# Optimization experiments

Hardware: AMD Instinct MI355X
Metric: run time of the kernel (lower is better)

The kernel has to match this reference:

```python
import jax, jax.numpy as jnp
import numpy as np

D_MODEL = 1024
NUM_HEADS = 16
HEAD_DIM = D_MODEL // NUM_HEADS


def setup_inputs() -> dict:
    key = jax.random.key(0)
    ks = jax.random.split(key, 10)
    B, SQ, SKV = 2, 2048, 2048
    s = 1.0 / np.sqrt(D_MODEL)
    inp = {
        "query": jax.random.normal(ks[0], (B, SQ, D_MODEL), jnp.float32),
        "key_value": jax.random.normal(ks[1], (B, SKV, D_MODEL), jnp.float32),
        "Wq": jax.random.normal(ks[2], (D_MODEL, D_MODEL), jnp.float32) * s,
        "bq": jnp.zeros((D_MODEL,), jnp.float32),
        "Wk": jax.random.normal(ks[3], (D_MODEL, D_MODEL), jnp.float32) * s,
        "bk": jnp.zeros((D_MODEL,), jnp.float32),
        "Wv": jax.random.normal(ks[4], (D_MODEL, D_MODEL), jnp.float32) * s,
        "bv": jnp.zeros((D_MODEL,), jnp.float32),
        "Wo": jax.random.normal(ks[5], (D_MODEL, D_MODEL), jnp.float32) * s,
        "bo": jnp.zeros((D_MODEL,), jnp.float32),
    }
    return inp


def reference(query, key_value, Wq, bq, Wk, bk, Wv, bv, Wo, bo):
    B, SQ, _ = query.shape
    SKV = key_value.shape[1]
    # projections (torch Linear: x @ W^T + b)
    Q = query @ Wq.T + bq
    K = key_value @ Wk.T + bk
    V = key_value @ Wv.T + bv
    # [B, H, S, Dh]
    Q = Q.reshape(B, SQ, NUM_HEADS, HEAD_DIM).transpose(0, 2, 1, 3)
    K = K.reshape(B, SKV, NUM_HEADS, HEAD_DIM).transpose(0, 2, 1, 3)
    V = V.reshape(B, SKV, NUM_HEADS, HEAD_DIM).transpose(0, 2, 1, 3)
    scores = jnp.einsum("bhqd,bhkd->bhqk", Q, K) / np.sqrt(HEAD_DIM)
    # causal mask: position q may attend to kv positions <= q
    causal = jnp.tril(jnp.ones((SQ, SKV), bool))  # True = keep
    scores = jnp.where(causal[None, None], scores, -jnp.inf)
    attn = jax.nn.softmax(scores, axis=-1)
    # dropout is identity in eval mode
    out = jnp.einsum("bhqk,bhkd->bhqd", attn, V)
    out = out.transpose(0, 2, 1, 3).reshape(B, SQ, D_MODEL)
    return out @ Wo.T + bo
```

## Files before the change

### kernel.cpp

```cpp
#include <hip/hip_runtime.h>
#include <hip/hip_bf16.h>
#include <cstdint>
#include <type_traits>

#define DM 1024
#define HEADS 16
#define DH 64
#define SEQ 2048
#define BATCH 2

typedef __attribute__((ext_vector_type(8))) short bf16x8;
typedef __attribute__((ext_vector_type(4))) float f32x4;
typedef __attribute__((ext_vector_type(16))) float f32x16;
typedef __attribute__((ext_vector_type(2))) unsigned int u32x2;
typedef __attribute__((ext_vector_type(4))) unsigned int u32x4;

#define SCALE2 0.18033688011112042f

#define GLOAD(dst, ptr) \
    asm volatile("global_load_dwordx4 %0, %1, off" : "=v"(dst) : "v"(ptr) : "memory")

static __device__ __forceinline__ unsigned short f2bf(float f) {
    unsigned u = __builtin_bit_cast(unsigned, f);
    u = u + 0x7fffu + ((u >> 16) & 1u);
    return (unsigned short)(u >> 16);
}
static __device__ __forceinline__ float bf2f(unsigned short us) {
    return __builtin_bit_cast(float, (unsigned)us << 16);
}

__global__ __launch_bounds__(256) void cast_all_k(
    const float* __restrict__ q, const float* __restrict__ kv,
    const float* __restrict__ wq, const float* __restrict__ wk,
    const float* __restrict__ wv, const float* __restrict__ wo,
    unsigned short* __restrict__ qb, unsigned short* __restrict__ kvb,
    unsigned short* __restrict__ wqb, unsigned short* __restrict__ wkb,
    unsigned short* __restrict__ wvb, unsigned short* __restrict__ wob)
{
    int blk = blockIdx.x;
    const float* s; unsigned short* d; int base;
    if (blk < 2048)      { s = q;  d = qb;  base = 0; }
    else if (blk < 4096) { s = kv; d = kvb; base = 2048; }
    else if (blk < 4608) { s = wq; d = wqb; base = 4096; }
    else if (blk < 5120) { s = wk; d = wkb; base = 4608; }
    else if (blk < 5632) { s = wv; d = wvb; base = 5120; }
    else                 { s = wo; d = wob; base = 5632; }
    int i = ((blk - base) * 256 + threadIdx.x) * 8;
    float4 a = *(const float4*)(s + i);
    float4 b2 = *(const float4*)(s + i + 4);
    ushort4 o0, o1;
    o0.x = f2bf(a.x);  o0.y = f2bf(a.y);  o0.z = f2bf(a.z);  o0.w = f2bf(a.w);
    o1.x = f2bf(b2.x); o1.y = f2bf(b2.y); o1.z = f2bf(b2.z); o1.w = f2bf(b2.w);
    *(ushort4*)(d + i) = o0;
    *(ushort4*)(d + i + 4) = o1;
}

template<int EPI>
__global__ __launch_bounds__(256) void gemm_nt(
    const unsigned short* __restrict__ A,
    const unsigned short* __restrict__ Bw,
    const float* __restrict__ biasA,
    const float* __restrict__ biasB,
    void* __restrict__ out0,
    void* __restrict__ out1,
    int M, int N, int K)
{
    constexpr int BK = 64;
    __shared__ alignas(16) unsigned short As[64 * BK];
    __shared__ alignas(16) unsigned short Bs[128 * BK];

    const int t = threadIdx.x;
    const int lane = t & 63;
    const int w = t >> 6;
    const int wn = w * 32;
    const int lr = lane & 15, lg = lane >> 4;
    const int m0 = blockIdx.x * 64, n0 = blockIdx.y * 128;

    f32x4 acc[4][2] = {};

    const int srow = t >> 3;
    const int schunk = t & 7;

    for (int kt = 0; kt < K; kt += BK) {
#pragma unroll
        for (int c = 0; c < 2; c++) {
            int row = srow + c * 32;
            int gc = schunk ^ (row & 7);
            __builtin_amdgcn_global_load_lds(
                (const __attribute__((address_space(1))) unsigned int*)(A + (size_t)(m0 + row) * K + kt + gc * 8),
                (__attribute__((address_space(3))) unsigned int*)(&As[row * BK + schunk * 8]), 16, 0, 0);
        }
#pragma unroll
        for (int c = 0; c < 4; c++) {
            int row = srow + c * 32;
            int gc = schunk ^ (row & 7);
            __builtin_amdgcn_global_load_lds(
                (const __attribute__((address_space(1))) unsigned int*)(Bw + (size_t)(n0 + row) * K + kt + gc * 8),
                (__attribute__((address_space(3))) unsigned int*)(&Bs[row * BK + schunk * 8]), 16, 0, 0);
        }
        __syncthreads();
#pragma unroll
        for (int kk = 0; kk < 2; kk++) {
            bf16x8 af[4], bfr[2];
#pragma unroll
            for (int i = 0; i < 4; i++)
                af[i] = *(const bf16x8*)(&As[(i * 16 + lr) * BK + (((kk * 4 + lg) ^ (lr & 7))) * 8]);
#pragma unroll
            for (int jj = 0; jj < 2; jj++)
                bfr[jj] = *(const bf16x8*)(&Bs[(wn + jj * 16 + lr) * BK + (((kk * 4 + lg) ^ (lr & 7))) * 8]);
#pragma unroll
            for (int i = 0; i < 4; i++)
#pragma unroll
                for (int jj = 0; jj < 2; jj++)
                    acc[i][jj] = __builtin_amdgcn_mfma_f32_16x16x32_bf16(af[i], bfr[jj], acc[i][jj], 0, 0, 0);
        }
        __syncthreads();
    }

    if constexpr (EPI == 0) {
        unsigned short* C = (unsigned short*)out0;
#pragma unroll
        for (int i = 0; i < 4; i++) {
            int rbase = m0 + i * 16 + lg * 4;
#pragma unroll
            for (int jj = 0; jj < 2; jj++) {
                int col = n0 + wn + jj * 16 + lr;
                float bv = biasA[col];
#pragma unroll
                for (int r = 0; r < 4; r++)
                    C[(size_t)(rbase + r) * 1024 + col] = f2bf((acc[i][jj][r] + bv) * SCALE2);
            }
        }
    } else if constexpr (EPI == 1) {
        if (n0 < 1024) {
            unsigned short* C = (unsigned short*)out0;
#pragma unroll
            for (int i = 0; i < 4; i++) {
                int rbase = m0 + i * 16 + lg * 4;
#pragma unroll
                for (int jj = 0; jj < 2; jj++) {
                    int col = n0 + wn + jj * 16 + lr;
                    float bv = biasA[col];
#pragma unroll
                    for (int r = 0; r < 4; r++)
                        C[(size_t)(rbase + r) * 1024 + col] = f2bf(acc[i][jj][r] + bv);
                }
            }
        } else {
            unsigned short* C = (unsigned short*)out1;
            int bidx = m0 >> 11;
#pragma unroll
            for (int i = 0; i < 4; i++) {
                int s0 = (m0 & 2047) + i * 16 + lg * 4;
#pragma unroll
                for (int jj = 0; jj < 2; jj++) {
                    int nv = n0 - 1024 + wn + jj * 16 + lr;
                    float bv = biasB[nv];
                    int hh = nv >> 6, dd = nv & 63;
                    ushort4 st;
                    st.x = f2bf(acc[i][jj][0] + bv);
                    st.y = f2bf(acc[i][jj][1] + bv);
                    st.z = f2bf(acc[i][jj][2] + bv);
                    st.w = f2bf(acc[i][jj][3] + bv);
                    *(ushort4*)(C + ((size_t)((bidx * HEADS + hh) * DH + dd)) * SEQ + s0) = st;
                }
            }
        }
    } else {
        float* C = (float*)out0;
#pragma unroll
        for (int i = 0; i < 4; i++) {
            int rbase = m0 + i * 16 + lg * 4;
#pragma unroll
            for (int jj = 0; jj < 2; jj++) {
                int col = n0 + wn + jj * 16 + lr;
                float bv = biasA[col];
#pragma unroll
                for (int r = 0; r < 4; r++)
                    C[(size_t)(rbase + r) * 1024 + col] = acc[i][jj][r] + bv;
            }
        }
    }
}

__global__ __launch_bounds__(256, 2) void attn_k(
    const unsigned short* __restrict__ Qp,
    const unsigned short* __restrict__ Kp,
    const unsigned short* __restrict__ Vt,
    unsigned short* __restrict__ Ctx,
    unsigned short* __restrict__ pO,
    float2* __restrict__ pML)
{
    __shared__ alignas(16) unsigned char ldsb[2 * 16384];

    const int lane = threadIdx.x & 63;
    const int w = threadIdx.x >> 6;
    const int x = blockIdx.x;
    const int bh = x & 31;
    const int g = x >> 5;
    int c, p, S;
    if (g < 4)       { c = g;                    p = 0;            S = 1; }
    else if (g < 12) { c = 4 + ((g - 4) >> 1);   p = (g - 4) & 1;  S = 2; }
    else if (g < 24) { c = 8 + (g - 12) / 3;     p = (g - 12) % 3; S = 3; }
    else             { c = 12 + ((g - 24) >> 2); p = (g - 24) & 3; S = 4; }
    const int nb = 2 * c + 2;
    const int len0 = (nb + S - 1) / S;
    const int start = p * len0;
    const int len = min(len0, nb - start);

    const int b = bh >> 4, h = bh & 15;
    const int q0 = c * 128;
    const int lq = lane & 31;
    const int hi = lane >> 5;
    const int qq = q0 + w * 32 + lq;
    const int my_nb = (q0 + 32 * w + 95) >> 6;
    constexpr float THR = 11.5f;

    bf16x8 Qf[4];
    {
        u32x4 qtmp[4];
        const unsigned short* qb = Qp + (size_t)(b * SEQ + qq) * DM + h * DH + hi * 8;
#pragma unroll
        for (int d = 0; d < 4; d++) GLOAD(qtmp[d], qb + d * 16);
        asm volatile("s_waitcnt vmcnt(0)" ::: "memory");
        __builtin_amdgcn_sched_barrier(0);
#pragma unroll
        for (int d = 0; d < 4; d++) Qf[d] = __builtin_bit_cast(bf16x8, qtmp[d]);
    }

    const int colx = (((lane & 7) ^ (lane >> 3)) << 4);
    const char* kg[2];
    const char* vg[2];
#pragma unroll
    for (int u = 0; u < 2; u++) {
        int s = 2 * w + u;
        int row = 8 * s + (lane >> 3);
        kg[u] = (const char*)Kp + (((size_t)(b * SEQ + row) * DM + h * DH) * 2) + colx;
        vg[u] = (const char*)Vt + ((((size_t)(b * HEADS + h) * DH + row) * SEQ) * 2) + colx;
    }
    const int kxor = (lq & 7) << 4;

    auto stage = [&](int buf, int t) {
        int kboff_k = t * (64 * DM * 2);
        int kboff_v = t * 128;
#pragma unroll
        for (int u = 0; u < 2; u++) {
            int s = 2 * w + u;
            __builtin_amdgcn_global_load_lds(
                (const __attribute__((address_space(1))) unsigned int*)(kg[u] + kboff_k),
                (__attribute__((address_space(3))) unsigned int*)(&ldsb[buf * 16384 + s * 1024 + lane * 16]), 16, 0, 0);
            __builtin_amdgcn_global_load_lds(
                (const __attribute__((address_space(1))) unsigned int*)(vg[u] + kboff_v),
                (__attribute__((address_space(3))) unsigned int*)(&ldsb[buf * 16384 + 8192 + s * 1024 + lane * 16]), 16, 0, 0);
        }
    };

    f32x16 o0 = {}, o1 = {};
    float m_run = -1e30f, l_run = 0.f;
    const int qmh0 = qq - 4 * hi;

    stage(0, start);

    for (int it = 0; it < len; it++) {
        const int t = start + it;
        const int cur = it & 1;
        if (it + 1 < len) {
            stage(cur ^ 1, t + 1);
            asm volatile("s_waitcnt vmcnt(4)" ::: "memory");
        } else {
            asm volatile("s_waitcnt vmcnt(0)" ::: "memory");
        }
        __builtin_amdgcn_sched_barrier(0);
        __builtin_amdgcn_s_barrier();

        if (t < my_nb) {
            const unsigned char* Kb = &ldsb[cur * 16384];
            const unsigned char* Vb = Kb + 8192;
            const int kb = t * 64;

            bf16x8 KA[4], KB[4], Vc[4][2];
#pragma unroll
            for (int d = 0; d < 4; d++) {
                int col = (d * 32 + hi * 16) ^ kxor;
                KA[d] = *(const bf16x8*)(Kb + lq * 128 + col);
                KB[d] = *(const bf16x8*)(Kb + (lq + 32) * 128 + col);
            }
#pragma unroll
            for (int s = 0; s < 4; s++)
#pragma unroll
                for (int dt = 0; dt < 2; dt++)
                    Vc[s][dt] = *(const bf16x8*)(Vb + (dt * 32 + lq) * 128 + ((s * 32 + hi * 16) ^ kxor));

            f32x16 sa0 = {}, sa1 = {};
            __builtin_amdgcn_s_setprio(1);
#pragma unroll
            for (int d = 0; d < 4; d++) {
                sa0 = __builtin_amdgcn_mfma_f32_32x32x16_bf16(KA[d], Qf[d], sa0, 0, 0, 0);
                sa1 = __builtin_amdgcn_mfma_f32_32x32x16_bf16(KB[d], Qf[d], sa1, 0, 0, 0);
            }
            __builtin_amdgcn_s_setprio(0);

            const int qmh = qmh0 - kb;
#pragma unroll
            for (int r = 0; r < 16; r++) {
                int kvl = (r & 3) + 8 * (r >> 2);
                sa0[r] = (kvl <= qmh) ? sa0[r] : -1e30f;
                sa1[r] = (kvl + 32 <= qmh) ? sa1[r] : -1e30f;
            }
            float mx[16];
#pragma unroll
            for (int r = 0; r < 16; r++) mx[r] = fmaxf(sa0[r], sa1[r]);
#pragma unroll
            for (int r = 0; r < 8; r++) mx[r] = fmaxf(mx[r], mx[r + 8]);
#pragma unroll
            for (int r = 0; r < 4; r++) mx[r] = fmaxf(mx[r], mx[r + 4]);
            mx[0] = fmaxf(mx[0], mx[2]);
            mx[1] = fmaxf(mx[1], mx[3]);
            float mloc = fmaxf(mx[0], mx[1]);
            mloc = fmaxf(mloc, __shfl_xor(mloc, 32));

            if (!__all(mloc - m_run <= THR)) {
                float m_new = fmaxf(m_run, mloc);
                float sf = __builtin_amdgcn_exp2f(m_run - m_new);
                l_run *= sf;
#pragma unroll
                for (int r = 0; r < 16; r++) { o0[r] *= sf; o1[r] *= sf; }
                m_run = m_new;
            }

            float p0v[16], p1v[16];
#pragma unroll
            for (int r = 0; r < 16; r++) {
                p0v[r] = __builtin_amdgcn_exp2f(sa0[r] - m_run);
                p1v[r] = __builtin_amdgcn_exp2f(sa1[r] - m_run);
            }
            float s4[8];
#pragma unroll
            for (int r = 0; r < 8; r++) s4[r] = (p0v[r] + p0v[r + 8]) + (p1v[r] + p1v[r + 8]);
#pragma unroll
            for (int r = 0; r < 4; r++) s4[r] += s4[r + 4];
            float ps = (s4[0] + s4[1]) + (s4[2] + s4[3]);
            ps += __shfl_xor(ps, 32);
            l_run += ps;

            unsigned c0[8], c1[8];
#pragma unroll
            for (int ii = 0; ii < 8; ii++) {
                unsigned pk;
                asm("v_cvt_pk_bf16_f32 %0, %1, %2" : "=v"(pk) : "v"(p0v[2 * ii]), "v"(p0v[2 * ii + 1]));
                c0[ii] = pk;
                asm("v_cvt_pk_bf16_f32 %0, %1, %2" : "=v"(pk) : "v"(p1v[2 * ii]), "v"(p1v[2 * ii + 1]));
                c1[ii] = pk;
            }
            bf16x8 Pb[4];
            {
                u32x2 r02 = __builtin_amdgcn_permlane32_swap(c0[0], c0[2], false, false);
                u32x2 r13 = __builtin_amdgcn_permlane32_swap(c0[1], c0[3], false, false);
                u32x2 r46 = __builtin_amdgcn_permlane32_swap(c0[4], c0[6], false, false);
                u32x2 r57 = __builtin_amdgcn_permlane32_swap(c0[5], c0[7], false, false);
                u32x4 w0 = {r02.x, r13.x, r02.y, r13.y};
                u32x4 w1 = {r46.x, r57.x, r46.y, r57.y};
                Pb[0] = __builtin_bit_cast(bf16x8, w0);
                Pb[1] = __builtin_bit_cast(bf16x8, w1);
            }
            {
                u32x2 r02 = __builtin_amdgcn_permlane32_swap(c1[0], c1[2], false, false);
                u32x2 r13 = __builtin_amdgcn_permlane32_swap(c1[1], c1[3], false, false);
                u32x2 r46 = __builtin_amdgcn_permlane32_swap(c1[4], c1[6], false, false);
                u32x2 r57 = __builtin_amdgcn_permlane32_swap(c1[5], c1[7], false, false);
                u32x4 w0 = {r02.x, r13.x, r02.y, r13.y};
                u32x4 w1 = {r46.x, r57.x, r46.y, r57.y};
                Pb[2] = __builtin_bit_cast(bf16x8, w0);
                Pb[3] = __builtin_bit_cast(bf16x8, w1);
            }

            __builtin_amdgcn_s_setprio(1);
#pragma unroll
            for (int s = 0; s < 4; s++) {
                o0 = __builtin_amdgcn_mfma_f32_32x32x16_bf16(Vc[s][0], Pb[s], o0, 0, 0, 0);
                o1 = __builtin_amdgcn_mfma_f32_32x32x16_bf16(Vc[s][1], Pb[s], o1, 0, 0, 0);
            }
            __builtin_amdgcn_s_setprio(0);
        }
        __builtin_amdgcn_s_barrier();
    }

    if (S == 1) {
        float inv = 1.0f / l_run;
        unsigned short* cb = Ctx + (size_t)(b * SEQ + qq) * DM + h * DH + hi * 4;
#pragma unroll
        for (int gg = 0; gg < 4; gg++) {
            ushort4 s0, s1;
            s0.x = f2bf(o0[4 * gg + 0] * inv); s0.y = f2bf(o0[4 * gg + 1] * inv);
            s0.z = f2bf(o0[4 * gg + 2] * inv); s0.w = f2bf(o0[4 * gg + 3] * inv);
            s1.x = f2bf(o1[4 * gg + 0] * inv); s1.y = f2bf(o1[4 * gg + 1] * inv);
            s1.z = f2bf(o1[4 * gg + 2] * inv); s1.w = f2bf(o1[4 * gg + 3] * inv);
            *(ushort4*)(cb + gg * 8) = s0;
            *(ushort4*)(cb + 32 + gg * 8) = s1;
        }
        return;
    }

    const int slot = g - 4;
    const int qrow = w * 32 + lq;
    unsigned short* pb = pO + ((size_t)(bh * 36 + slot) * 8192) + qrow * 64 + hi * 4;
#pragma unroll
    for (int gg = 0; gg < 4; gg++) {
        ushort4 s0, s1;
        s0.x = f2bf(o0[4 * gg + 0]); s0.y = f2bf(o0[4 * gg + 1]);
        s0.z = f2bf(o0[4 * gg + 2]); s0.w = f2bf(o0[4 * gg + 3]);
        s1.x = f2bf(o1[4 * gg + 0]); s1.y = f2bf(o1[4 * gg + 1]);
        s1.z = f2bf(o1[4 * gg + 2]); s1.w = f2bf(o1[4 * gg + 3]);
        *(ushort4*)(pb + gg * 8) = s0;
        *(ushort4*)(pb + 32 + gg * 8) = s1;
    }
    if (hi == 0)
        pML[(size_t)(bh * 36 + slot) * 128 + qrow] = make_float2(m_run, l_run);
}

__global__ __launch_bounds__(256) void combine_k(
    const unsigned short* __restrict__ pO,
    const float2* __restrict__ pML,
    unsigned short* __restrict__ Ctx)
{
    const int x = blockIdx.x;
    const int bh = x & 31;
    const int c = (x >> 5) + 4;
    const int S = (c >> 2) + 1;
    int slot0;
    if (c < 8)       slot0 = 2 * (c - 4);
    else if (c < 12) slot0 = 8 + 3 * (c - 8);
    else             slot0 = 20 + 4 * (c - 12);
    const int b = bh >> 4, h = bh & 15;

    const int q = threadIdx.x >> 1;
    const int d0 = (threadIdx.x & 1) * 32;

    float m[4], l[4], wgt[4];
    float M = -1e30f;
#pragma unroll
    for (int i = 0; i < 4; i++) {
        if (i < S) {
            float2 ml = pML[(size_t)(bh * 36 + slot0 + i) * 128 + q];
            m[i] = ml.x; l[i] = ml.y;
            M = fmaxf(M, m[i]);
        }
    }
    float L = 0.f;
#pragma unroll
    for (int i = 0; i < 4; i++) {
        if (i < S) {
            wgt[i] = __builtin_amdgcn_exp2f(m[i] - M);
            L += l[i] * wgt[i];
        }
    }
    float invL = 1.0f / L;
#pragma unroll
    for (int i = 0; i < 4; i++) if (i < S) wgt[i] *= invL;

    unsigned short* cb = Ctx + (size_t)(b * SEQ + c * 128 + q) * DM + h * DH + d0;
#pragma unroll
    for (int dd = 0; dd < 32; dd += 8) {
        float acc[8] = {};
#pragma unroll
        for (int i = 0; i < 4; i++) {
            if (i < S) {
                const unsigned short* pp = pO + ((size_t)(bh * 36 + slot0 + i) * 8192) + q * 64 + d0 + dd;
                bf16x8 v = *(const bf16x8*)pp;
#pragma unroll
                for (int e = 0; e < 8; e++)
                    acc[e] += wgt[i] * bf2f((unsigned short)v[e]);
            }
        }
        ushort4 s0, s1;
        s0.x = f2bf(acc[0]); s0.y = f2bf(acc[1]); s0.z = f2bf(acc[2]); s0.w = f2bf(acc[3]);
        s1.x = f2bf(acc[4]); s1.y = f2bf(acc[5]); s1.z = f2bf(acc[6]); s1.w = f2bf(acc[7]);
        *(ushort4*)(cb + dd) = s0;
        *(ushort4*)(cb + dd + 4) = s1;
    }
}

extern "C" void kernel_launch(void* const* d_in, const int* in_sizes, int n_in,
                              void* d_out, int out_size, void* d_ws, size_t ws_size,
                              hipStream_t stream)
{
    const float* query = (const float*)d_in[0];
    const float* keyv  = (const float*)d_in[1];
    const float* Wq = (const float*)d_in[2];
    const float* bq = (const float*)d_in[3];
    const float* Wk = (const float*)d_in[4];
    const float* bk = (const float*)d_in[5];
    const float* Wv = (const float*)d_in[6];
    const float* bv = (const float*)d_in[7];
    const float* Wo = (const float*)d_in[8];
    const float* bo = (const float*)d_in[9];
    float* out = (float*)d_out;

    const int M = BATCH * SEQ;
    char* ws = (char*)d_ws;
    size_t off = 0;
    auto alloc = [&](size_t elems) { unsigned short* p = (unsigned short*)(ws + off); off += elems * 2; return p; };
    unsigned short* qb  = alloc((size_t)M * DM);
    unsigned short* kvb = alloc((size_t)M * DM);
    unsigned short* wqb = alloc((size_t)DM * DM);
    unsigned short* wkb = alloc((size_t)DM * DM);
    unsigned short* wvb = alloc((size_t)DM * DM);
    unsigned short* wob = alloc((size_t)DM * DM);
    unsigned short* Qp  = alloc((size_t)M * DM);
    unsigned short* Kp  = alloc((size_t)M * DM);
    unsigned short* Vt  = alloc((size_t)M * DM);
    unsigned short* Ctx = alloc((size_t)M * DM);

    unsigned short* pO  = (unsigned short*)(ws + 0);
    float2*         pML = (float2*)(ws + 20971520);

    cast_all_k<<<6144, 256, 0, stream>>>(query, keyv, Wq, Wk, Wv, Wo,
                                         qb, kvb, wqb, wkb, wvb, wob);

    gemm_nt<0><<<dim3(M / 64, 8),  256, 0, stream>>>(qb,  wqb, bq, nullptr, Qp, nullptr, M, DM, DM);
    gemm_nt<1><<<dim3(M / 64, 16), 256, 0, stream>>>(kvb, wkb, bk, bv,      Kp, Vt,      M, 2 * DM, DM);

    attn_k<<<dim3(1280), 256, 0, stream>>>(Qp, Kp, Vt, Ctx, pO, pML);
    combine_k<<<dim3(384), 256, 0, stream>>>(pO, pML, Ctx);

    gemm_nt<2><<<dim3(M / 64, 8),  256, 0, stream>>>(Ctx, wob, bo, nullptr, out, nullptr, M, DM, DM);
}
```

Measured before the change: 122.3 us.

## Double-buffer GEMM LDS tiles and skip causal masking on fully visible blocks

The projection GEMM now keeps two LDS buffers and issues the global-to-LDS loads for the next K tile before computing on the current one. A partial vmcnt wait replaces the full sync, so load latency can overlap with MFMA work. Separately, the attention kernel applies the per-element causal mask only on KV blocks that cross the diagonal, which saves ALU selects on interior blocks. The costs are doubled LDS use in the GEMM, which may lower occupancy, and a hand-tuned vmcnt count that has to match the number of loads issued.

```diff
diff --git a/kernel.cpp b/kernel.cpp
--- a/kernel.cpp
+++ b/kernel.cpp
@@ -66,8 +66,8 @@
     int M, int N, int K)
 {
     constexpr int BK = 64;
-    __shared__ alignas(16) unsigned short As[64 * BK];
-    __shared__ alignas(16) unsigned short Bs[128 * BK];
+    __shared__ alignas(16) unsigned short As[2][64 * BK];
+    __shared__ alignas(16) unsigned short Bs[2][128 * BK];
 
     const int t = threadIdx.x;
     const int lane = t & 63;
@@ -81,14 +81,14 @@
     const int srow = t >> 3;
     const int schunk = t & 7;
 
-    for (int kt = 0; kt < K; kt += BK) {
+    auto stageG = [&](int buf, int kt) {
 #pragma unroll
         for (int c = 0; c < 2; c++) {
             int row = srow + c * 32;
             int gc = schunk ^ (row & 7);
             __builtin_amdgcn_global_load_lds(
                 (const __attribute__((address_space(1))) unsigned int*)(A + (size_t)(m0 + row) * K + kt + gc * 8),
-                (__attribute__((address_space(3))) unsigned int*)(&As[row * BK + schunk * 8]), 16, 0, 0);
+                (__attribute__((address_space(3))) unsigned int*)(&As[buf][row * BK + schunk * 8]), 16, 0, 0);
         }
 #pragma unroll
         for (int c = 0; c < 4; c++) {
@@ -96,25 +96,39 @@
             int gc = schunk ^ (row & 7);
             __builtin_amdgcn_global_load_lds(
                 (const __attribute__((address_space(1))) unsigned int*)(Bw + (size_t)(n0 + row) * K + kt + gc * 8),
-                (__attribute__((address_space(3))) unsigned int*)(&Bs[row * BK + schunk * 8]), 16, 0, 0);
-        }
-        __syncthreads();
+                (__attribute__((address_space(3))) unsigned int*)(&Bs[buf][row * BK + schunk * 8]), 16, 0, 0);
+        }
+    };
+
+    const int nkt = K / BK;
+    stageG(0, 0);
+
+    for (int ki = 0; ki < nkt; ki++) {
+        const int cur = ki & 1;
+        if (ki + 1 < nkt) {
+            stageG(cur ^ 1, (ki + 1) * BK);
+            asm volatile("s_waitcnt vmcnt(6)" ::: "memory");
+        } else {
+            asm volatile("s_waitcnt vmcnt(0)" ::: "memory");
+        }
+        __builtin_amdgcn_sched_barrier(0);
+        __builtin_amdgcn_s_barrier();
 #pragma unroll
         for (int kk = 0; kk < 2; kk++) {
             bf16x8 af[4], bfr[2];
 #pragma unroll
             for (int i = 0; i < 4; i++)
-                af[i] = *(const bf16x8*)(&As[(i * 16 + lr) * BK + (((kk * 4 + lg) ^ (lr & 7))) * 8]);
+                af[i] = *(const bf16x8*)(&As[cur][(i * 16 + lr) * BK + (((kk * 4 + lg) ^ (lr & 7))) * 8]);
 #pragma unroll
             for (int jj = 0; jj < 2; jj++)
-                bfr[jj] = *(const bf16x8*)(&Bs[(wn + jj * 16 + lr) * BK + (((kk * 4 + lg) ^ (lr & 7))) * 8]);
+                bfr[jj] = *(const bf16x8*)(&Bs[cur][(wn + jj * 16 + lr) * BK + (((kk * 4 + lg) ^ (lr & 7))) * 8]);
 #pragma unroll
             for (int i = 0; i < 4; i++)
 #pragma unroll
                 for (int jj = 0; jj < 2; jj++)
                     acc[i][jj] = __builtin_amdgcn_mfma_f32_16x16x32_bf16(af[i], bfr[jj], acc[i][jj], 0, 0, 0);
         }
-        __syncthreads();
+        __builtin_amdgcn_s_barrier();
     }
 
     if constexpr (EPI == 0) {
@@ -214,6 +228,7 @@
     const int hi = lane >> 5;
     const int qq = q0 + w * 32 + lq;
     const int my_nb = (q0 + 32 * w + 95) >> 6;
+    const int qmin = q0 + 32 * w;
     constexpr float THR = 11.5f;
 
     bf16x8 Qf[4];
@@ -300,12 +315,14 @@
             }
             __builtin_amdgcn_s_setprio(0);
 
-            const int qmh = qmh0 - kb;
-#pragma unroll
-            for (int r = 0; r < 16; r++) {
-                int kvl = (r & 3) + 8 * (r >> 2);
-                sa0[r] = (kvl <= qmh) ? sa0[r] : -1e30f;
-                sa1[r] = (kvl + 32 <= qmh) ? sa1[r] : -1e30f;
+            if (kb + 63 > qmin) {
+                const int qmh = qmh0 - kb;
+#pragma unroll
+                for (int r = 0; r < 16; r++) {
+                    int kvl = (r & 3) + 8 * (r >> 2);
+                    sa0[r] = (kvl <= qmh) ? sa0[r] : -1e30f;
+                    sa1[r] = (kvl + 32 <= qmh) ? sa1[r] : -1e30f;
+                }
             }
             float mx[16];
 #pragma unroll
```

Measured after the change: 124.3 us. Within noise of the previous version (+1.7%).
